# Performance work log

Measured on AMD Instinct MI355X. Metric: run time of the kernel, lower is better.

The kernel has to match this reference:

```python
import jax, jax.numpy as jnp
import numpy as np

N, E, H, MID = 4096, 384, 6, 96  # n_refs, embed_dim, num_heads, mlp mid dim (max(E//4,32))
DH = E // H  # head dim = 64


def setup_inputs() -> dict:
    key = jax.random.key(0)
    ks = jax.random.split(key, 12)
    def w(k, shape, fan_in):
        return jax.random.normal(k, shape, jnp.float32) / np.float32(np.sqrt(fan_in))
    return {
        "low": jax.random.normal(ks[0], (N, E), jnp.float32),
        "high": jax.random.normal(ks[1], (N, E), jnp.float32),
        "ref_w": jax.random.uniform(ks[2], (N,), jnp.float32) + 0.1,
        "low_w1": w(ks[3], (E, MID), E), "low_b1": jnp.zeros((MID,), jnp.float32),
        "low_w2": w(ks[4], (MID, E), MID), "low_b2": jnp.zeros((E,), jnp.float32),
        "high_w1": w(ks[5], (E, MID), E), "high_b1": jnp.zeros((MID,), jnp.float32),
        "high_w2": w(ks[6], (MID, E), MID), "high_b2": jnp.zeros((E,), jnp.float32),
        "layer_fuse": jnp.array([0.4, 0.6], jnp.float32),
        "wqkv": w(ks[7], (E, 3 * E), E), "bqkv": jnp.zeros((3 * E,), jnp.float32),
        "wo": w(ks[8], (E, E), E), "bo": jnp.zeros((E,), jnp.float32),
        "ln_g": jnp.ones((E,), jnp.float32), "ln_b": jnp.zeros((E,), jnp.float32),
    }


def _channel_mlp(x, w1, b1, w2, b2):
    h = jax.nn.gelu(x @ w1 + b1, approximate=False)  # [N, MID]
    return x * jax.nn.sigmoid(h @ w2 + b2)           # [N, E]


def _forward(low, high, ref_w, low_w1, low_b1, low_w2, low_b2,
             high_w1, high_b1, high_w2, high_b2, layer_fuse,
             wqkv, bqkv, wo, bo, ln_g, ln_b):
    lw = jax.nn.softmax(layer_fuse)
    fused = lw[0] * _channel_mlp(low, low_w1, low_b1, low_w2, low_b2) \
          + lw[1] * _channel_mlp(high, high_w1, high_b1, high_w2, high_b2)  # [N, E]
    # single-layer MHA over the n-reference sequence (batch of 1, batch_first)
    qkv = fused @ wqkv + bqkv                      # [N, 3E]
    q, k, v = jnp.split(qkv, 3, axis=-1)
    q = q.reshape(N, H, DH).transpose(1, 0, 2)     # [H, N, DH]
    k = k.reshape(N, H, DH).transpose(1, 0, 2)
    v = v.reshape(N, H, DH).transpose(1, 0, 2)
    scores = jnp.einsum("hnd,hmd->hnm", q, k) / np.float32(np.sqrt(DH))
    attn = jax.nn.softmax(scores, axis=-1)         # [H, N, N]
    ctx = jnp.einsum("hnm,hmd->hnd", attn, v)      # [H, N, DH]
    attn_out = ctx.transpose(1, 0, 2).reshape(N, E) @ wo + bo
    x = attn_out + fused                           # residual
    mu = jnp.mean(x, axis=-1, keepdims=True)
    var = jnp.mean(jnp.square(x - mu), axis=-1, keepdims=True)
    x = (x - mu) / jnp.sqrt(var + 1e-5) * ln_g + ln_b
    w = ref_w / jnp.sum(ref_w)
    res = jnp.sum(x * w[:, None], axis=0)          # weighted mean over refs -> [E]
    return res / (jnp.linalg.norm(res) + 1e-8)


def reference(low, high, ref_w, low_w1, low_b1, low_w2, low_b2,
              high_w1, high_b1, high_w2, high_b2, layer_fuse,
              wqkv, bqkv, wo, bo, ln_g, ln_b):
    return _forward(low, high, ref_w, low_w1, low_b1, low_w2, low_b2,
                    high_w1, high_b1, high_w2, high_b2, layer_fuse,
                    wqkv, bqkv, wo, bo, ln_g, ln_b)
```

## Files before the change

kernel.cpp:

```cpp
#include <hip/hip_runtime.h>
#include <math.h>

#define Nn 4096
#define Ee 384
#define Hh 6
#define DHh 64
#define MIDm 96
#define TEe 1152
#define SPLIT 8

typedef short s16x8 __attribute__((ext_vector_type(8)));
typedef float f32x4 __attribute__((ext_vector_type(4)));
typedef float f32x16 __attribute__((ext_vector_type(16)));
typedef unsigned short ushort_t;
typedef unsigned short ushort4_t __attribute__((ext_vector_type(4)));

#define CROW(r, hf) ((((r) & 3)) + 8 * ((r) >> 2) + 4 * (hf))

__device__ __forceinline__ float gelu_exact(float x) {
    return 0.5f * x * (1.0f + erff(x * 0.70710678118654752f));
}
__device__ __forceinline__ float sigmoidf_(float x) {
    return 1.0f / (1.0f + __expf(-x));
}
__device__ __forceinline__ ushort_t f2bf(float x) {
    unsigned int u = __float_as_uint(x);
    u = (u + 0x7FFFu + ((u >> 16) & 1u)) >> 16;
    return (ushort_t)u;
}
__device__ __forceinline__ float bf2f(ushort_t u) {
    return __uint_as_float(((unsigned int)u) << 16);
}
__device__ __forceinline__ unsigned int cvtpk(float a, float b) {
    unsigned int r;
    asm("v_cvt_pk_bf16_f32 %0, %1, %2" : "=v"(r) : "v"(a), "v"(b));
    return r;
}
__device__ __forceinline__ void gld16(const ushort_t* g, ushort_t* l) {
    __builtin_amdgcn_global_load_lds(
        (const __attribute__((address_space(1))) unsigned int*)g,
        (__attribute__((address_space(3))) unsigned int*)l, 16, 0, 0);
}

#define W1L_OFF 0
#define W1H_OFF 36864
#define W2L_OFF 73728
#define W2H_OFF 110592
#define WQKV_OFF 147456
#define WO_OFF 589824

__global__ __launch_bounds__(256) void k_cvt(
    const float* __restrict__ lw1, const float* __restrict__ hw1,
    const float* __restrict__ lw2, const float* __restrict__ hw2,
    const float* __restrict__ wqkv, const float* __restrict__ wo,
    ushort_t* __restrict__ wT) {
    __shared__ float tl[32][33];
    const int b = blockIdx.x;
    const float* src;
    int R, C, doff, ti;
    if (b < 36)       { src = lw1;  R = 384; C = 96;   doff = W1L_OFF;  ti = b; }
    else if (b < 72)  { src = hw1;  R = 384; C = 96;   doff = W1H_OFF;  ti = b - 36; }
    else if (b < 108) { src = lw2;  R = 96;  C = 384;  doff = W2L_OFF;  ti = b - 72; }
    else if (b < 144) { src = hw2;  R = 96;  C = 384;  doff = W2H_OFF;  ti = b - 108; }
    else if (b < 576) { src = wqkv; R = 384; C = 1152; doff = WQKV_OFF; ti = b - 144; }
    else              { src = wo;   R = 384; C = 384;  doff = WO_OFF;   ti = b - 576; }
    const int tcn = C >> 5;
    const int tr = ti / tcn, tc = ti % tcn;
    const int col = threadIdx.x & 31, r8 = threadIdx.x >> 5;
#pragma unroll
    for (int i = 0; i < 4; i++) {
        const int row = r8 + 8 * i;
        tl[row][col] = src[(size_t)(tr * 32 + row) * C + tc * 32 + col];
    }
    __syncthreads();
#pragma unroll
    for (int i = 0; i < 4; i++) {
        const int rowp = r8 + 8 * i;
        wT[doff + (size_t)(tc * 32 + rowp) * R + tr * 32 + col] = f2bf(tl[col][rowp]);
    }
}

__global__ __launch_bounds__(256) void k_mlp(
    const float* __restrict__ low, const float* __restrict__ high,
    const float* __restrict__ lf, const ushort_t* __restrict__ wT,
    const float* __restrict__ lb1, const float* __restrict__ lb2,
    const float* __restrict__ hb1, const float* __restrict__ hb2,
    ushort_t* __restrict__ fusedb) {
    __shared__ float redsg[6144];
    __shared__ ushort_t Hs[2][16][104];
    float* red = redsg;
    ushort_t* Sg = (ushort_t*)redsg;
    const int t = threadIdx.x;
    const int w = t >> 6, l = t & 63, l15 = l & 15, g4 = l >> 4;
    const int st = w >> 1, kh = w & 1;
    const int rb = blockIdx.x * 16;
    const float* Xf = st ? high : low;
    const ushort_t* w1T = wT + (st ? W1H_OFF : W1L_OFF);
    const ushort_t* w2T = wT + (st ? W2H_OFF : W2L_OFF);
    {
        f32x4 hA[6];
#pragma unroll
        for (int nt = 0; nt < 6; nt++) hA[nt] = (f32x4){0.f, 0.f, 0.f, 0.f};
        for (int ks = 0; ks < 6; ks++) {
            const float* ap = &Xf[(size_t)(rb + l15) * 384 + kh * 192 + ks * 32 + g4 * 8];
            f32x4 a0 = *(const f32x4*)ap;
            f32x4 a1 = *(const f32x4*)(ap + 4);
            union { unsigned int uw[4]; s16x8 v; } ua;
            ua.uw[0] = cvtpk(a0[0], a0[1]);
            ua.uw[1] = cvtpk(a0[2], a0[3]);
            ua.uw[2] = cvtpk(a1[0], a1[1]);
            ua.uw[3] = cvtpk(a1[2], a1[3]);
#pragma unroll
            for (int nt = 0; nt < 6; nt++) {
                s16x8 bf = *(const s16x8*)&w1T[(nt * 16 + l15) * 384 + kh * 192 + ks * 32 + g4 * 8];
                hA[nt] = __builtin_amdgcn_mfma_f32_16x16x32_bf16(ua.v, bf, hA[nt], 0, 0, 0);
            }
        }
#pragma unroll
        for (int nt = 0; nt < 6; nt++)
#pragma unroll
            for (int r = 0; r < 4; r++)
                red[((st * 2 + kh) * 16 + g4 * 4 + r) * 96 + nt * 16 + l15] = hA[nt][r];
    }
    __syncthreads();
    for (int idx = t; idx < 2 * 16 * 96; idx += 256) {
        const int st2 = idx / 1536, rem = idx % 1536;
        const int rowm = rem / 96, mc = rem % 96;
        const float v = red[((st2 * 2) * 16 + rowm) * 96 + mc] +
                        red[((st2 * 2 + 1) * 16 + rowm) * 96 + mc] +
                        (st2 ? hb1[mc] : lb1[mc]);
        Hs[st2][rowm][mc] = f2bf(gelu_exact(v));
    }
    __syncthreads();
    {
        const float* b2p = st ? hb2 : lb2;
        f32x4 sA[12];
#pragma unroll
        for (int nt = 0; nt < 12; nt++) sA[nt] = (f32x4){0.f, 0.f, 0.f, 0.f};
#pragma unroll
        for (int ks = 0; ks < 3; ks++) {
            s16x8 af = *(const s16x8*)&Hs[st][l15][ks * 32 + g4 * 8];
#pragma unroll
            for (int nt = 0; nt < 12; nt++) {
                s16x8 bf = *(const s16x8*)&w2T[(kh * 192 + nt * 16 + l15) * 96 + ks * 32 + g4 * 8];
                sA[nt] = __builtin_amdgcn_mfma_f32_16x16x32_bf16(af, bf, sA[nt], 0, 0, 0);
            }
        }
#pragma unroll
        for (int nt = 0; nt < 12; nt++) {
            const float bb = b2p[kh * 192 + nt * 16 + l15];
#pragma unroll
            for (int r = 0; r < 4; r++)
                Sg[(st * 16 + g4 * 4 + r) * 384 + kh * 192 + nt * 16 + l15] =
                    f2bf(sigmoidf_(sA[nt][r] + bb));
        }
    }
    __syncthreads();
    {
        const float a0 = lf[0], a1 = lf[1];
        const float mx = fmaxf(a0, a1);
        const float e0 = __expf(a0 - mx), e1 = __expf(a1 - mx);
        const float inv = 1.0f / (e0 + e1);
        const float w0 = e0 * inv, w1v = e1 * inv;
        for (int base = t * 4; base < 16 * 384; base += 256 * 4) {
            const int row = base / 384, e0i = base % 384;
            const int gr = rb + row;
            f32x4 lo4 = *(const f32x4*)&low[(size_t)gr * 384 + e0i];
            f32x4 hi4 = *(const f32x4*)&high[(size_t)gr * 384 + e0i];
            ushort4_t s0 = *(const ushort4_t*)&Sg[row * 384 + e0i];
            ushort4_t s1 = *(const ushort4_t*)&Sg[(16 + row) * 384 + e0i];
            ushort4_t fb;
#pragma unroll
            for (int i = 0; i < 4; i++)
                fb[i] = f2bf(w0 * lo4[i] * bf2f(s0[i]) + w1v * hi4[i] * bf2f(s1[i]));
            *(ushort4_t*)&fusedb[(size_t)gr * 384 + e0i] = fb;
        }
    }
}

__global__ __launch_bounds__(128) void k_qkv(
    const ushort_t* __restrict__ fusedb, const ushort_t* __restrict__ wT,
    const float* __restrict__ bqkv,
    ushort_t* __restrict__ qb, ushort_t* __restrict__ kb, ushort_t* __restrict__ vtb) {
    __shared__ float tls[2][32][40];
    const int t = threadIdx.x;
    const int w = t >> 6, l = t & 63, ll = l & 31, hf = l >> 5;
    const int rb = blockIdx.x * 32;
    const int cb = blockIdx.y * 192 + w * 96;
    const ushort_t* wq = wT + WQKV_OFF;
    f32x16 acc[3];
#pragma unroll
    for (int nt = 0; nt < 3; nt++)
#pragma unroll
        for (int r = 0; r < 16; r++) acc[nt][r] = 0.0f;
    for (int ks = 0; ks < 24; ks++) {
        s16x8 af = *(const s16x8*)&fusedb[(size_t)(rb + ll) * 384 + ks * 16 + hf * 8];
#pragma unroll
        for (int nt = 0; nt < 3; nt++) {
            s16x8 bf = *(const s16x8*)&wq[(size_t)(cb + nt * 32 + ll) * 384 + ks * 16 + hf * 8];
            acc[nt] = __builtin_amdgcn_mfma_f32_32x32x16_bf16(af, bf, acc[nt], 0, 0, 0);
        }
    }
#pragma unroll
    for (int nt = 0; nt < 3; nt++) {
        const int nb = cb + nt * 32;
        const int which = nb / 384, wn = nb % 384;
        const int hb = wn >> 6, d0 = wn & 63;
        const float bias = bqkv[nb + ll];
        if (which == 2) {
            const int d = d0 + ll;
#pragma unroll
            for (int g2 = 0; g2 < 4; g2++) {
                ushort4_t u4;
#pragma unroll
                for (int i2 = 0; i2 < 4; i2++) u4[i2] = f2bf(acc[nt][g2 * 4 + i2] + bias);
                *(ushort4_t*)&vtb[((size_t)(hb * 64 + d)) * Nn + rb + 8 * g2 + 4 * hf] = u4;
            }
        } else {
            const float sc = (which == 0) ? 0.18033688f : 1.0f;
#pragma unroll
            for (int r = 0; r < 16; r++) tls[w][CROW(r, hf)][ll] = (acc[nt][r] + bias) * sc;
            ushort_t* dst = which ? kb : qb;
            const int row2 = l >> 1, sg = l & 1;
            union { ushort_t us[16]; s16x8 v[2]; } u;
#pragma unroll
            for (int j = 0; j < 16; j++) u.us[j] = f2bf(tls[w][row2][sg * 16 + j]);
            size_t base = ((size_t)hb * Nn + rb + row2) * 64 + d0 + sg * 16;
            *(s16x8*)&dst[base] = u.v[0];
            *(s16x8*)&dst[base + 8] = u.v[1];
        }
    }
}

__global__ __launch_bounds__(512) void k_attn(
    const ushort_t* __restrict__ qb, const ushort_t* __restrict__ kb,
    const ushort_t* __restrict__ vtb, ushort_t* __restrict__ pof,
    float* __restrict__ pml) {
    __shared__ ushort_t Kt[2][4096];
    __shared__ ushort_t Vt[2][4096];
    const int t = threadIdx.x;
    const int wid8 = t >> 6, l = t & 63, ll = l & 31, hf = l >> 5;
    const int lid = blockIdx.x;
    const int xcd = lid & 7, gi = lid >> 3;
    const int pair = xcd * 6 + (gi >> 4);
    const int qt = gi & 15;
    const int h = pair % Hh, sp = pair / Hh;
    const int qrow0 = qt * 256 + wid8 * 32;
    const int srow = t >> 3;
    const int sslot = ((l & 7) ^ (l >> 3)) * 8;
    const int wch = wid8 * 512;
    const ushort_t* kbase = kb + (size_t)h * Nn * DHh;
    const ushort_t* vbase = vtb + (size_t)h * DHh * Nn;
    const int kst0 = sp * (Nn / SPLIT);
#define NT (Nn / (64 * SPLIT))
#define STAGE(B, TI) { const int ktb2 = kst0 + (TI) * 64;                                \
        gld16(kbase + (size_t)(ktb2 + srow) * DHh + sslot, &Kt[B][wch]);                 \
        gld16(vbase + (size_t)srow * Nn + ktb2 + sslot, &Vt[B][wch]); }

    s16x8 qf[4];
#pragma unroll
    for (int dc = 0; dc < 4; dc++)
        qf[dc] = *(const s16x8*)&qb[((size_t)h * Nn + qrow0 + ll) * DHh + dc * 16 + hf * 8];
    f32x16 zro;
#pragma unroll
    for (int r = 0; r < 16; r++) zro[r] = 0.0f;
    f32x16 o0 = zro, o1 = zro;
    float lsum = 0.0f;
    const int xorl = (ll & 7) << 3;

    STAGE(0, 0);
    __syncthreads();
    for (int kt = 0; kt < NT; kt++) {
        const int cur = kt & 1;
        if (kt < NT - 1) STAGE(cur ^ 1, kt + 1);
        const ushort_t* KtC = Kt[cur];
        const ushort_t* VtC = Vt[cur];
        __builtin_amdgcn_s_setprio(1);
        f32x16 s0, s1;
        {
            const int colE = hf * 8;
            s16x8 kf0 = *(const s16x8*)&KtC[ll * 64 + (colE ^ xorl)];
            s16x8 kf1 = *(const s16x8*)&KtC[(32 + ll) * 64 + (colE ^ xorl)];
            s0 = __builtin_amdgcn_mfma_f32_32x32x16_bf16(kf0, qf[0], zro, 0, 0, 0);
            s1 = __builtin_amdgcn_mfma_f32_32x32x16_bf16(kf1, qf[0], zro, 0, 0, 0);
        }
#pragma unroll
        for (int dc = 1; dc < 4; dc++) {
            const int colE = dc * 16 + hf * 8;
            s16x8 kf0 = *(const s16x8*)&KtC[ll * 64 + (colE ^ xorl)];
            s16x8 kf1 = *(const s16x8*)&KtC[(32 + ll) * 64 + (colE ^ xorl)];
            s0 = __builtin_amdgcn_mfma_f32_32x32x16_bf16(kf0, qf[dc], s0, 0, 0, 0);
            s1 = __builtin_amdgcn_mfma_f32_32x32x16_bf16(kf1, qf[dc], s1, 0, 0, 0);
        }
        __builtin_amdgcn_s_setprio(0);
#pragma unroll
        for (int r = 0; r < 16; r++) { s0[r] = exp2f(s0[r]); lsum += s0[r]; }
#pragma unroll
        for (int r = 0; r < 16; r++) { s1[r] = exp2f(s1[r]); lsum += s1[r]; }
#pragma unroll
        for (int ks = 0; ks < 4; ks++) {
            const f32x16 S = (ks < 2) ? s0 : s1;
            const int b = (ks & 1) * 8;
            unsigned int t1 = cvtpk(S[b + 0], S[b + 1]);
            unsigned int t3 = cvtpk(S[b + 2], S[b + 3]);
            unsigned int t2 = cvtpk(S[b + 4], S[b + 5]);
            unsigned int t4 = cvtpk(S[b + 6], S[b + 7]);
            asm("v_permlane32_swap_b32 %0, %1" : "+v"(t1), "+v"(t2));
            asm("v_permlane32_swap_b32 %0, %1" : "+v"(t3), "+v"(t4));
            union { unsigned int uw[4]; s16x8 v; } u;
            u.uw[0] = t1;
            u.uw[1] = t3;
            u.uw[2] = t2;
            u.uw[3] = t4;
            const int colE = ks * 16 + hf * 8;
            s16x8 vf0 = *(const s16x8*)&VtC[ll * 64 + (colE ^ xorl)];
            s16x8 vf1 = *(const s16x8*)&VtC[(32 + ll) * 64 + (colE ^ xorl)];
            o0 = __builtin_amdgcn_mfma_f32_32x32x16_bf16(vf0, u.v, o0, 0, 0, 0);
            o1 = __builtin_amdgcn_mfma_f32_32x32x16_bf16(vf1, u.v, o1, 0, 0, 0);
        }
        __syncthreads();
    }
    lsum += __shfl_xor(lsum, 32, 64);
    const size_t bq = ((size_t)sp * 256 + (qrow0 >> 4) + (ll >> 4)) * 384;
    const int q15 = ll & 15;
#pragma unroll
    for (int r = 0; r < 16; r++) {
        const int e_a = h * 64 + CROW(r, hf);
        pof[(bq + e_a) * 16 + q15] = f2bf(o0[r]);
        pof[(bq + e_a + 32) * 16 + q15] = f2bf(o1[r]);
    }
    if (hf == 0)
        pml[((size_t)sp * Hh + h) * Nn + qrow0 + ll] = lsum;
#undef STAGE
#undef NT
}

__global__ __launch_bounds__(512) void k_oln(
    const ushort_t* __restrict__ pof, const float* __restrict__ pml,
    const ushort_t* __restrict__ wT, const float* __restrict__ bo,
    const ushort_t* __restrict__ fusedb,
    const float* __restrict__ lng, const float* __restrict__ lnb,
    const float* __restrict__ rw, float* __restrict__ part) {
    __shared__ ushort_t cx[16][384];
    __shared__ float xs[16][388];
    __shared__ float stats[16][2];
    __shared__ float dinvs[Hh][16];
    const int t = threadIdx.x;
    const int w = t >> 6, l = t & 63, l15 = l & 15, g4 = l >> 4;
    const int rb = blockIdx.x * 16;
    const int rbq = blockIdx.x;
    if (t < Hh * 16) {
        const int hh = t >> 4, qq = t & 15;
        float den = 0.0f;
#pragma unroll
        for (int s = 0; s < SPLIT; s++)
            den += pml[((size_t)s * Hh + hh) * Nn + rb + qq];
        dinvs[hh][qq] = 1.0f / den;
    }
    __syncthreads();
    for (int task = t; task < 768; task += 512) {
        const int e = task >> 1, half = task & 1;
        const int hh = e >> 6;
        float a8[8];
#pragma unroll
        for (int j = 0; j < 8; j++) a8[j] = 0.0f;
#pragma unroll
        for (int s = 0; s < SPLIT; s++) {
            s16x8 v = *(const s16x8*)&pof[(((size_t)s * 256 + rbq) * 384 + e) * 16 + half * 8];
#pragma unroll
            for (int j = 0; j < 8; j++) a8[j] += bf2f((ushort_t)v[j]);
        }
#pragma unroll
        for (int j = 0; j < 8; j++) {
            const int q = half * 8 + j;
            cx[q][e ^ ((q & 7) << 3)] = f2bf(a8[j] * dinvs[hh][q]);
        }
    }
    __syncthreads();
    const ushort_t* woT = wT + WO_OFF;
    f32x4 oA[3];
#pragma unroll
    for (int nt = 0; nt < 3; nt++) oA[nt] = (f32x4){0.f, 0.f, 0.f, 0.f};
    const int xo = (l15 & 7) << 3;
    for (int ks = 0; ks < 12; ks++) {
        s16x8 af = *(const s16x8*)&cx[l15][(ks * 32 + g4 * 8) ^ xo];
#pragma unroll
        for (int nt = 0; nt < 3; nt++) {
            s16x8 bf = *(const s16x8*)&woT[(size_t)(w * 48 + nt * 16 + l15) * 384 + ks * 32 + g4 * 8];
            oA[nt] = __builtin_amdgcn_mfma_f32_16x16x32_bf16(af, bf, oA[nt], 0, 0, 0);
        }
    }
#pragma unroll
    for (int nt = 0; nt < 3; nt++) {
        const int col = w * 48 + nt * 16 + l15;
        const float bias = bo[col];
#pragma unroll
        for (int r = 0; r < 4; r++) {
            const int row = g4 * 4 + r;
            xs[row][col] = oA[nt][r] + bias + bf2f(fusedb[(size_t)(rb + row) * 384 + col]);
        }
    }
    __syncthreads();
    {
        const int row = t >> 5, j = t & 31;
        float s1 = 0.0f, s2 = 0.0f;
        for (int i = 0; i < 12; i++) {
            const float x = xs[row][j + 32 * i];
            s1 += x;
            s2 += x * x;
        }
#pragma unroll
        for (int off = 1; off < 32; off <<= 1) {
            s1 += __shfl_xor(s1, off, 64);
            s2 += __shfl_xor(s2, off, 64);
        }
        if (j == 0) {
            const float mu = s1 * (1.0f / Ee);
            const float var = s2 * (1.0f / Ee) - mu * mu;
            stats[row][0] = mu;
            stats[row][1] = rsqrtf(var + 1e-5f);
        }
    }
    __syncthreads();
    for (int c = t; c < 384; c += 512) {
        const float gt = lng[c], bb = lnb[c];
        float acc = 0.0f;
        for (int r = 0; r < 16; r++) {
            const float xn = (xs[r][c] - stats[r][0]) * stats[r][1] * gt + bb;
            acc += xn * rw[rb + r];
        }
        part[(size_t)blockIdx.x * Ee + c] = acc;
    }
}

__global__ __launch_bounds__(384) void k_final(const float* __restrict__ part,
                                               const float* __restrict__ rw,
                                               float* __restrict__ outp) {
    __shared__ float red[6], redw[6];
    const int t = threadIdx.x;
    float s = 0.0f;
    for (int b = 0; b < 256; b++) s += part[(size_t)b * Ee + t];
    float wsp = 0.0f;
    for (int i = t; i < Nn; i += 384) wsp += rw[i];
    float q2 = s * s;
#pragma unroll
    for (int off = 32; off > 0; off >>= 1) {
        q2 += __shfl_down(q2, off, 64);
        wsp += __shfl_down(wsp, off, 64);
    }
    const int wid = t >> 6, lane = t & 63;
    if (lane == 0) { red[wid] = q2; redw[wid] = wsp; }
    __syncthreads();
    float tot = 0.0f, wtot = 0.0f;
#pragma unroll
    for (int w = 0; w < 6; w++) { tot += red[w]; wtot += redw[w]; }
    outp[t] = s / (sqrtf(tot) + 1e-8f * wtot);
}

extern "C" void kernel_launch(void* const* d_in, const int* in_sizes, int n_in,
                              void* d_out, int out_size, void* d_ws, size_t ws_size,
                              hipStream_t stream) {
    const float* low  = (const float*)d_in[0];
    const float* high = (const float*)d_in[1];
    const float* rw   = (const float*)d_in[2];
    const float* lw1  = (const float*)d_in[3];
    const float* lb1  = (const float*)d_in[4];
    const float* lw2  = (const float*)d_in[5];
    const float* lb2  = (const float*)d_in[6];
    const float* hw1  = (const float*)d_in[7];
    const float* hb1  = (const float*)d_in[8];
    const float* hw2  = (const float*)d_in[9];
    const float* hb2  = (const float*)d_in[10];
    const float* lf   = (const float*)d_in[11];
    const float* wqkv = (const float*)d_in[12];
    const float* bqkv = (const float*)d_in[13];
    const float* wo   = (const float*)d_in[14];
    const float* bo   = (const float*)d_in[15];
    const float* lng  = (const float*)d_in[16];
    const float* lnb  = (const float*)d_in[17];

    float* ws = (float*)d_ws;
    const size_t NE = (size_t)Nn * Ee;
    float* pml  = ws;
    float* part = ws + 196608;
    ushort_t* u16base = (ushort_t*)(ws + 294912);
    ushort_t* fusedb = u16base;
    ushort_t* vtb    = u16base + NE;
    ushort_t* qb     = u16base + 2 * NE;
    ushort_t* kb     = u16base + 3 * NE;
    ushort_t* wT     = u16base + 4 * NE;
    ushort_t* pof    = wT + 737280;

    hipLaunchKernelGGL(k_cvt, dim3(720), dim3(256), 0, stream,
                       lw1, hw1, lw2, hw2, wqkv, wo, wT);
    hipLaunchKernelGGL(k_mlp, dim3(256), dim3(256), 0, stream,
                       low, high, lf, wT, lb1, lb2, hb1, hb2, fusedb);
    hipLaunchKernelGGL(k_qkv, dim3(128, 6), dim3(128), 0, stream,
                       fusedb, wT, bqkv, qb, kb, vtb);
    hipLaunchKernelGGL(k_attn, dim3(Hh * SPLIT * 16), dim3(512), 0, stream,
                       qb, kb, vtb, pof, pml);
    hipLaunchKernelGGL(k_oln, dim3(256), dim3(512), 0, stream,
                       pof, pml, wT, bo, fusedb, lng, lnb, rw, part);
    hipLaunchKernelGGL(k_final, dim3(1), dim3(384), 0, stream, part, rw, (float*)d_out);
}
```

Before: 125.0 us.

## Split channel MLP into two kernels and transpose partial-sum layout

The fused channel-MLP kernel is split in two. The first kernel computes the GELU hidden layer per stream over the full K dimension with a 2D grid, which removes the split-K shared-memory reduction; the second kernel computes the sigmoid gate and the fused output. The hidden activations now make a round trip through a global bf16 buffer, and the pipeline gains one extra launch. The per-block partials from the LayerNorm stage are stored column-major, so the final reduction can read them with contiguous float4 loads.

```diff
diff --git a/kernel.cpp b/kernel.cpp
--- a/kernel.cpp
+++ b/kernel.cpp
@@ -80,101 +80,102 @@
     }
 }
 
-__global__ __launch_bounds__(256) void k_mlp(
+__global__ __launch_bounds__(128) void k_mlp1(
     const float* __restrict__ low, const float* __restrict__ high,
-    const float* __restrict__ lf, const ushort_t* __restrict__ wT,
-    const float* __restrict__ lb1, const float* __restrict__ lb2,
-    const float* __restrict__ hb1, const float* __restrict__ hb2,
-    ushort_t* __restrict__ fusedb) {
-    __shared__ float redsg[6144];
-    __shared__ ushort_t Hs[2][16][104];
-    float* red = redsg;
-    ushort_t* Sg = (ushort_t*)redsg;
+    const ushort_t* __restrict__ wT,
+    const float* __restrict__ lb1, const float* __restrict__ hb1,
+    ushort_t* __restrict__ Hb) {
+    __shared__ ushort_t Hs[16][96];
     const int t = threadIdx.x;
     const int w = t >> 6, l = t & 63, l15 = l & 15, g4 = l >> 4;
-    const int st = w >> 1, kh = w & 1;
     const int rb = blockIdx.x * 16;
+    const int st = blockIdx.y;
     const float* Xf = st ? high : low;
     const ushort_t* w1T = wT + (st ? W1H_OFF : W1L_OFF);
+    const float* b1p = st ? hb1 : lb1;
+    f32x4 hA[3];
+#pragma unroll
+    for (int nt = 0; nt < 3; nt++) hA[nt] = (f32x4){0.f, 0.f, 0.f, 0.f};
+    for (int ks = 0; ks < 12; ks++) {
+        const float* ap = &Xf[(size_t)(rb + l15) * 384 + ks * 32 + g4 * 8];
+        f32x4 a0 = *(const f32x4*)ap;
+        f32x4 a1 = *(const f32x4*)(ap + 4);
+        union { unsigned int uw[4]; s16x8 v; } ua;
+        ua.uw[0] = cvtpk(a0[0], a0[1]);
+        ua.uw[1] = cvtpk(a0[2], a0[3]);
+        ua.uw[2] = cvtpk(a1[0], a1[1]);
+        ua.uw[3] = cvtpk(a1[2], a1[3]);
+#pragma unroll
+        for (int nt = 0; nt < 3; nt++) {
+            s16x8 bf = *(const s16x8*)&w1T[(w * 48 + nt * 16 + l15) * 384 + ks * 32 + g4 * 8];
+            hA[nt] = __builtin_amdgcn_mfma_f32_16x16x32_bf16(ua.v, bf, hA[nt], 0, 0, 0);
+        }
+    }
+#pragma unroll
+    for (int nt = 0; nt < 3; nt++) {
+        const int mc = w * 48 + nt * 16 + l15;
+        const float bb = b1p[mc];
+#pragma unroll
+        for (int r = 0; r < 4; r++)
+            Hs[g4 * 4 + r][mc] = f2bf(gelu_exact(hA[nt][r] + bb));
+    }
+    __syncthreads();
+    for (int i = t; i < 192; i += 128) {
+        const int row = i / 12, c8 = i % 12;
+        *(s16x8*)&Hb[((size_t)st * Nn + rb + row) * 96 + c8 * 8] = *(const s16x8*)&Hs[row][c8 * 8];
+    }
+}
+
+__global__ __launch_bounds__(256) void k_mlp2(
+    const float* __restrict__ low, const float* __restrict__ high,
+    const ushort_t* __restrict__ Hb, const float* __restrict__ lf,
+    const ushort_t* __restrict__ wT,
+    const float* __restrict__ lb2, const float* __restrict__ hb2,
+    ushort_t* __restrict__ fusedb) {
+    __shared__ ushort_t Sg[2][16][384];
+    const int t = threadIdx.x;
+    const int w = t >> 6, l = t & 63, l15 = l & 15, g4 = l >> 4;
+    const int st = w >> 1, nh = w & 1;
+    const int rb = blockIdx.x * 16;
     const ushort_t* w2T = wT + (st ? W2H_OFF : W2L_OFF);
-    {
-        f32x4 hA[6];
-#pragma unroll
-        for (int nt = 0; nt < 6; nt++) hA[nt] = (f32x4){0.f, 0.f, 0.f, 0.f};
-        for (int ks = 0; ks < 6; ks++) {
-            const float* ap = &Xf[(size_t)(rb + l15) * 384 + kh * 192 + ks * 32 + g4 * 8];
-            f32x4 a0 = *(const f32x4*)ap;
-            f32x4 a1 = *(const f32x4*)(ap + 4);
-            union { unsigned int uw[4]; s16x8 v; } ua;
-            ua.uw[0] = cvtpk(a0[0], a0[1]);
-            ua.uw[1] = cvtpk(a0[2], a0[3]);
-            ua.uw[2] = cvtpk(a1[0], a1[1]);
-            ua.uw[3] = cvtpk(a1[2], a1[3]);
-#pragma unroll
-            for (int nt = 0; nt < 6; nt++) {
-                s16x8 bf = *(const s16x8*)&w1T[(nt * 16 + l15) * 384 + kh * 192 + ks * 32 + g4 * 8];
-                hA[nt] = __builtin_amdgcn_mfma_f32_16x16x32_bf16(ua.v, bf, hA[nt], 0, 0, 0);
-            }
-        }
-#pragma unroll
-        for (int nt = 0; nt < 6; nt++)
-#pragma unroll
-            for (int r = 0; r < 4; r++)
-                red[((st * 2 + kh) * 16 + g4 * 4 + r) * 96 + nt * 16 + l15] = hA[nt][r];
-    }
-    __syncthreads();
-    for (int idx = t; idx < 2 * 16 * 96; idx += 256) {
-        const int st2 = idx / 1536, rem = idx % 1536;
-        const int rowm = rem / 96, mc = rem % 96;
-        const float v = red[((st2 * 2) * 16 + rowm) * 96 + mc] +
-                        red[((st2 * 2 + 1) * 16 + rowm) * 96 + mc] +
-                        (st2 ? hb1[mc] : lb1[mc]);
-        Hs[st2][rowm][mc] = f2bf(gelu_exact(v));
-    }
-    __syncthreads();
-    {
-        const float* b2p = st ? hb2 : lb2;
-        f32x4 sA[12];
-#pragma unroll
-        for (int nt = 0; nt < 12; nt++) sA[nt] = (f32x4){0.f, 0.f, 0.f, 0.f};
-#pragma unroll
-        for (int ks = 0; ks < 3; ks++) {
-            s16x8 af = *(const s16x8*)&Hs[st][l15][ks * 32 + g4 * 8];
-#pragma unroll
-            for (int nt = 0; nt < 12; nt++) {
-                s16x8 bf = *(const s16x8*)&w2T[(kh * 192 + nt * 16 + l15) * 96 + ks * 32 + g4 * 8];
-                sA[nt] = __builtin_amdgcn_mfma_f32_16x16x32_bf16(af, bf, sA[nt], 0, 0, 0);
-            }
-        }
+    const float* b2p = st ? hb2 : lb2;
+    f32x4 sA[12];
+#pragma unroll
+    for (int nt = 0; nt < 12; nt++) sA[nt] = (f32x4){0.f, 0.f, 0.f, 0.f};
+#pragma unroll
+    for (int ks = 0; ks < 3; ks++) {
+        s16x8 af = *(const s16x8*)&Hb[((size_t)st * Nn + rb + l15) * 96 + ks * 32 + g4 * 8];
 #pragma unroll
         for (int nt = 0; nt < 12; nt++) {
-            const float bb = b2p[kh * 192 + nt * 16 + l15];
-#pragma unroll
-            for (int r = 0; r < 4; r++)
-                Sg[(st * 16 + g4 * 4 + r) * 384 + kh * 192 + nt * 16 + l15] =
-                    f2bf(sigmoidf_(sA[nt][r] + bb));
-        }
-    }
-    __syncthreads();
-    {
-        const float a0 = lf[0], a1 = lf[1];
-        const float mx = fmaxf(a0, a1);
-        const float e0 = __expf(a0 - mx), e1 = __expf(a1 - mx);
-        const float inv = 1.0f / (e0 + e1);
-        const float w0 = e0 * inv, w1v = e1 * inv;
-        for (int base = t * 4; base < 16 * 384; base += 256 * 4) {
-            const int row = base / 384, e0i = base % 384;
-            const int gr = rb + row;
-            f32x4 lo4 = *(const f32x4*)&low[(size_t)gr * 384 + e0i];
-            f32x4 hi4 = *(const f32x4*)&high[(size_t)gr * 384 + e0i];
-            ushort4_t s0 = *(const ushort4_t*)&Sg[row * 384 + e0i];
-            ushort4_t s1 = *(const ushort4_t*)&Sg[(16 + row) * 384 + e0i];
-            ushort4_t fb;
-#pragma unroll
-            for (int i = 0; i < 4; i++)
-                fb[i] = f2bf(w0 * lo4[i] * bf2f(s0[i]) + w1v * hi4[i] * bf2f(s1[i]));
-            *(ushort4_t*)&fusedb[(size_t)gr * 384 + e0i] = fb;
-        }
+            s16x8 bf = *(const s16x8*)&w2T[(nh * 192 + nt * 16 + l15) * 96 + ks * 32 + g4 * 8];
+            sA[nt] = __builtin_amdgcn_mfma_f32_16x16x32_bf16(af, bf, sA[nt], 0, 0, 0);
+        }
+    }
+#pragma unroll
+    for (int nt = 0; nt < 12; nt++) {
+        const float bb = b2p[nh * 192 + nt * 16 + l15];
+#pragma unroll
+        for (int r = 0; r < 4; r++)
+            Sg[st][g4 * 4 + r][nh * 192 + nt * 16 + l15] = f2bf(sigmoidf_(sA[nt][r] + bb));
+    }
+    __syncthreads();
+    const float a0 = lf[0], a1 = lf[1];
+    const float mx = fmaxf(a0, a1);
+    const float e0 = __expf(a0 - mx), e1 = __expf(a1 - mx);
+    const float inv = 1.0f / (e0 + e1);
+    const float w0 = e0 * inv, w1v = e1 * inv;
+    for (int base = t * 4; base < 16 * 384; base += 256 * 4) {
+        const int row = base / 384, e0i = base % 384;
+        const int gr = rb + row;
+        f32x4 lo4 = *(const f32x4*)&low[(size_t)gr * 384 + e0i];
+        f32x4 hi4 = *(const f32x4*)&high[(size_t)gr * 384 + e0i];
+        ushort4_t s0 = *(const ushort4_t*)&Sg[0][row][e0i];
+        ushort4_t s1 = *(const ushort4_t*)&Sg[1][row][e0i];
+        ushort4_t fb;
+#pragma unroll
+        for (int i = 0; i < 4; i++)
+            fb[i] = f2bf(w0 * lo4[i] * bf2f(s0[i]) + w1v * hi4[i] * bf2f(s1[i]));
+        *(ushort4_t*)&fusedb[(size_t)gr * 384 + e0i] = fb;
     }
 }
 
@@ -429,7 +430,7 @@
             const float xn = (xs[r][c] - stats[r][0]) * stats[r][1] * gt + bb;
             acc += xn * rw[rb + r];
         }
-        part[(size_t)blockIdx.x * Ee + c] = acc;
+        part[(size_t)c * 256 + rbq] = acc;
     }
 }
 
@@ -439,7 +440,10 @@
     __shared__ float red[6], redw[6];
     const int t = threadIdx.x;
     float s = 0.0f;
-    for (int b = 0; b < 256; b++) s += part[(size_t)b * Ee + t];
+    for (int b4 = 0; b4 < 64; b4++) {
+        f32x4 v = *(const f32x4*)&part[(size_t)t * 256 + b4 * 4];
+        s += v[0] + v[1] + v[2] + v[3];
+    }
     float wsp = 0.0f;
     for (int i = t; i < Nn; i += 384) wsp += rw[i];
     float q2 = s * s;
@@ -489,12 +493,15 @@
     ushort_t* qb     = u16base + 2 * NE;
     ushort_t* kb     = u16base + 3 * NE;
     ushort_t* wT     = u16base + 4 * NE;
-    ushort_t* pof    = wT + 737280;
+    ushort_t* Hb     = wT + 737280;
+    ushort_t* pof    = Hb + 786432;
 
     hipLaunchKernelGGL(k_cvt, dim3(720), dim3(256), 0, stream,
                        lw1, hw1, lw2, hw2, wqkv, wo, wT);
-    hipLaunchKernelGGL(k_mlp, dim3(256), dim3(256), 0, stream,
-                       low, high, lf, wT, lb1, lb2, hb1, hb2, fusedb);
+    hipLaunchKernelGGL(k_mlp1, dim3(256, 2), dim3(128), 0, stream,
+                       low, high, wT, lb1, hb1, Hb);
+    hipLaunchKernelGGL(k_mlp2, dim3(256), dim3(256), 0, stream,
+                       low, high, Hb, lf, wT, lb2, hb2, fusedb);
     hipLaunchKernelGGL(k_qkv, dim3(128, 6), dim3(128), 0, stream,
                        fusedb, wT, bqkv, qb, kb, vtb);
     hipLaunchKernelGGL(k_attn, dim3(Hh * SPLIT * 16), dim3(512), 0, stream,
```

After: 130.7 us. 1.05x slower.
